# Optimization experiments

Hardware: AMD Instinct MI355X
Metric: run time of the kernel (lower is better)

Reference implementation:

```python
import jax, jax.numpy as jnp
import numpy as np

TOP_K = 2
B, S, H, I, E = 1, 2048, 1024, 4096, 8


def setup_inputs() -> dict:
    key = jax.random.key(0)
    k1, k2, k3, k4 = jax.random.split(key, 4)
    x = jax.random.normal(k1, (B, S, H), dtype=jnp.float32)
    gate_w = jax.random.normal(k2, (E, H), dtype=jnp.float32)
    w1 = jax.random.normal(k3, (E, I, H), dtype=jnp.float32)
    w2 = jax.random.normal(k4, (E, H, I), dtype=jnp.float32)
    return {"x": x, "gate_w": gate_w, "w1": w1, "w2": w2}


def reference(x, gate_w, w1, w2):
    b, s, h = x.shape
    xf = x.reshape(-1, h)                      # [T, H]
    T = xf.shape[0]
    logits = xf @ gate_w.T                     # [T, E]
    probs = jax.nn.softmax(logits, axis=-1)
    wts, idx = jax.lax.top_k(probs, TOP_K)     # [T, k]
    wts = wts / jnp.sum(wts, axis=-1, keepdims=True)
    # combine[t, e] = routing weight of expert e for token t (0 if not selected)
    combine = jnp.zeros((T, w1.shape[0]), dtype=x.dtype)
    combine = combine.at[jnp.arange(T)[:, None], idx].add(wts)
    # dense dispatch: every expert processes every token, masked/weighted by combine
    hid = jax.nn.silu(jnp.einsum('th,eih->tei', xf, w1))   # [T, E, I]
    y = jnp.einsum('tei,ehi->teh', hid, w2)                # [T, E, H]
    out = jnp.einsum('teh,te->th', y, combine)             # [T, H]
    return out.reshape(b, s, h)
```

## Files before the change

### kernel.cpp

```cpp
#include <hip/hip_runtime.h>
#include <stdint.h>

#define TT 2048
#define HH 1024
#define II 4096
#define EE 8
#define KS 4

typedef __attribute__((ext_vector_type(4))) float floatx4;
typedef __attribute__((ext_vector_type(8))) __bf16 bf16x8;

__device__ __forceinline__ unsigned short f2bf(float f) {
  union { float f; unsigned u; } v; v.f = f;
  return (unsigned short)((v.u + 0x7FFFu + ((v.u >> 16) & 1u)) >> 16);
}

__device__ __forceinline__ void async_ld16(const void* g, void* l) {
  __builtin_amdgcn_global_load_lds(
      (__attribute__((address_space(1))) void*)g,
      (__attribute__((address_space(3))) void*)l, 16, 0, 0);
}

__global__ __launch_bounds__(256) void k_gating(
    const float* __restrict__ x, const float* __restrict__ gw,
    unsigned short* __restrict__ xb, int* __restrict__ sel_e,
    float* __restrict__ sel_w, int* __restrict__ counts) {
  int t = blockIdx.x;
  int tid = threadIdx.x;
  floatx4 xv = ((const floatx4*)(x + (size_t)t * HH))[tid];
  ushort4 xo;
  xo.x = f2bf(xv.x); xo.y = f2bf(xv.y); xo.z = f2bf(xv.z); xo.w = f2bf(xv.w);
  ((ushort4*)(xb + (size_t)t * HH))[tid] = xo;

  float part[EE];
#pragma unroll
  for (int e = 0; e < EE; e++) {
    floatx4 g = ((const floatx4*)(gw + e * HH))[tid];
    part[e] = xv.x * g.x + xv.y * g.y + xv.z * g.z + xv.w * g.w;
  }
#pragma unroll
  for (int e = 0; e < EE; e++) {
    float v = part[e];
#pragma unroll
    for (int off = 32; off > 0; off >>= 1) v += __shfl_down(v, off, 64);
    part[e] = v;
  }
  __shared__ float red[4][EE];
  int wave = tid >> 6;
  if ((tid & 63) == 0) {
#pragma unroll
    for (int e = 0; e < EE; e++) red[wave][e] = part[e];
  }
  __syncthreads();
  if (tid == 0) {
    float lg[EE];
#pragma unroll
    for (int e = 0; e < EE; e++)
      lg[e] = red[0][e] + red[1][e] + red[2][e] + red[3][e];
    int e0 = 0;
#pragma unroll
    for (int e = 1; e < EE; e++) if (lg[e] > lg[e0]) e0 = e;
    int e1 = (e0 == 0) ? 1 : 0;
#pragma unroll
    for (int e = 0; e < EE; e++) if (e != e0 && lg[e] > lg[e1]) e1 = e;
    float w0 = 1.f / (1.f + expf(lg[e1] - lg[e0]));
    sel_e[t * 2] = e0; sel_e[t * 2 + 1] = e1;
    sel_w[t * 2] = w0; sel_w[t * 2 + 1] = 1.f - w0;
    atomicAdd(&counts[e0], 1);
    atomicAdd(&counts[e1], 1);
  }
}

__global__ __launch_bounds__(256) void k_fill(
    const int* __restrict__ counts, const int* __restrict__ sel_e,
    const float* __restrict__ sel_w, int* __restrict__ bases,
    int* __restrict__ row_token, float* __restrict__ row_w,
    int* __restrict__ inv_slot) {
  __shared__ int lb[EE];
  __shared__ int lc[EE];
  int tid = threadIdx.x;
  if (tid == 0) {
    int s = 0;
    for (int e = 0; e < EE; e++) { lb[e] = s; s += counts[e]; }
  }
  if (tid < EE) lc[tid] = 0;
  __syncthreads();
  for (int p = tid; p < TT * 2; p += 256) {
    int e = sel_e[p];
    int slot = lb[e] + atomicAdd(&lc[e], 1);
    row_token[slot] = p >> 1;
    row_w[slot] = sel_w[p];
    inv_slot[p] = slot;
  }
  __syncthreads();
  if (tid < EE) bases[tid] = lb[tid];
}

__global__ __launch_bounds__(256) void k_gemm1(
    const unsigned short* __restrict__ xb,
    const float* __restrict__ w1,
    unsigned short* __restrict__ hid,
    const int* __restrict__ counts, const int* __restrict__ bases,
    const int* __restrict__ row_token) {
  const int e = blockIdx.z;
  const int count = counts[e];
  const int m0 = blockIdx.y * 128;
  if (m0 >= count) return;
  const int n0 = blockIdx.x * 128;
  const int base = bases[e];

  __shared__ __align__(16) unsigned short Smem[128 * 32 * 2];
  unsigned short* As = Smem;
  unsigned short* Bs = Smem + 128 * 32;

  const int tid = threadIdx.x;
  const int lane = tid & 63;
  const int wave = tid >> 6;
  const int wm = (wave & 1) * 64;
  const int wn = (wave >> 1) * 64;
  const int quad = lane >> 4;
  const int l16 = lane & 15;

  const int rA0 = tid >> 2;
  const int rA1 = rA0 + 64;
  const int cc = (tid & 3) * 8;

  int g0 = m0 + rA0; if (g0 > count - 1) g0 = count - 1;
  int g1 = m0 + rA1; if (g1 > count - 1) g1 = count - 1;
  const unsigned short* aS0 = xb + (size_t)row_token[base + g0] * HH + cc;
  const unsigned short* aS1 = xb + (size_t)row_token[base + g1] * HH + cc;
  const float* wp = w1 + (size_t)e * II * HH;
  const float* bp0 = wp + (size_t)(n0 + rA0) * HH + cc;
  const float* bp1 = wp + (size_t)(n0 + rA1) * HH + cc;

  unsigned short* lA0 = As + tid * 8;
  unsigned short* lA1 = As + tid * 8 + 2048;
  unsigned short* lB0 = Bs + tid * 8;
  unsigned short* lB1 = Bs + tid * 8 + 2048;

  const floatx4 fz = {0.f, 0.f, 0.f, 0.f};
  floatx4 acc[4][4];
#pragma unroll
  for (int i = 0; i < 4; i++)
#pragma unroll
    for (int j = 0; j < 4; j++) acc[i][j] = fz;

  floatx4 f0a = *(const floatx4*)(bp0);
  floatx4 f0b = *(const floatx4*)(bp0 + 4);
  floatx4 f1a = *(const floatx4*)(bp1);
  floatx4 f1b = *(const floatx4*)(bp1 + 4);

  for (int k0 = 0; k0 < HH; k0 += 32) {
    bf16x8 wv0, wv1;
#pragma unroll
    for (int j = 0; j < 4; j++) {
      wv0[j] = (__bf16)f0a[j]; wv0[j + 4] = (__bf16)f0b[j];
      wv1[j] = (__bf16)f1a[j]; wv1[j + 4] = (__bf16)f1b[j];
    }
    *(bf16x8*)lB0 = wv0;
    *(bf16x8*)lB1 = wv1;
    async_ld16(aS0 + k0, lA0);
    async_ld16(aS1 + k0, lA1);
    __syncthreads();
    if (k0 + 32 < HH) {
      f0a = *(const floatx4*)(bp0 + k0 + 32);
      f0b = *(const floatx4*)(bp0 + k0 + 36);
      f1a = *(const floatx4*)(bp1 + k0 + 32);
      f1b = *(const floatx4*)(bp1 + k0 + 36);
    }
    bf16x8 af[4], bfr[4];
#pragma unroll
    for (int i = 0; i < 4; i++) {
      af[i]  = *(const bf16x8*)(As + (wm + i * 16 + l16) * 32 + quad * 8);
      bfr[i] = *(const bf16x8*)(Bs + (wn + i * 16 + l16) * 32 + quad * 8);
    }
#pragma unroll
    for (int i = 0; i < 4; i++)
#pragma unroll
      for (int j = 0; j < 4; j++)
        acc[i][j] = __builtin_amdgcn_mfma_f32_16x16x32_bf16(af[i], bfr[j], acc[i][j], 0, 0, 0);
    __syncthreads();
  }

  unsigned short* Sl = Smem + wave * (16 * 72);
#pragma unroll
  for (int i = 0; i < 4; i++) {
#pragma unroll
    for (int r = 0; r < 4; r++) {
      const int row16 = quad * 4 + r;
#pragma unroll
      for (int j = 0; j < 4; j++) {
        float z = acc[i][j][r];
        Sl[row16 * 72 + l16 + 16 * j] = f2bf(z / (1.f + __expf(-z)));
      }
    }
#pragma unroll
    for (int half = 0; half < 2; half++) {
      const int row16 = (lane >> 3) + 8 * half;
      const int m = wm + i * 16 + row16;
      if (m0 + m < count) {
        bf16x8 v = *(const bf16x8*)(Sl + row16 * 72 + (lane & 7) * 8);
        *(bf16x8*)(hid + (size_t)(base + m0 + m) * II + n0 + wn + (lane & 7) * 8) = v;
      }
    }
  }
}

__global__ __launch_bounds__(256) void k_gemm2(
    const unsigned short* __restrict__ hid,
    const float* __restrict__ w2,
    float* __restrict__ yp,
    const int* __restrict__ counts, const int* __restrict__ bases) {
  const int e = blockIdx.z;
  const int count = counts[e];
  const int m0 = blockIdx.y * 128;
  if (m0 >= count) return;
  const int nt = blockIdx.x & 7;
  const int ks = blockIdx.x >> 3;
  const int n0 = nt * 128;
  const int base = bases[e];

  __shared__ __align__(16) unsigned short Smem2[128 * 32 * 2];
  unsigned short* As = Smem2;
  unsigned short* Bs = Smem2 + 128 * 32;

  const int tid = threadIdx.x;
  const int lane = tid & 63;
  const int wave = tid >> 6;
  const int wm = (wave & 1) * 64;
  const int wn = (wave >> 1) * 64;
  const int quad = lane >> 4;
  const int l16 = lane & 15;

  const int rA0 = tid >> 2;
  const int rA1 = rA0 + 64;
  const int cc = (tid & 3) * 8;

  int g0 = m0 + rA0; if (g0 > count - 1) g0 = count - 1;
  int g1 = m0 + rA1; if (g1 > count - 1) g1 = count - 1;
  const unsigned short* aS0 = hid + (size_t)(base + g0) * II + cc;
  const unsigned short* aS1 = hid + (size_t)(base + g1) * II + cc;
  const float* wp = w2 + (size_t)e * HH * II;
  const float* bp0 = wp + (size_t)(n0 + rA0) * II + cc;
  const float* bp1 = wp + (size_t)(n0 + rA1) * II + cc;

  unsigned short* lA0 = As + tid * 8;
  unsigned short* lA1 = As + tid * 8 + 2048;
  unsigned short* lB0 = Bs + tid * 8;
  unsigned short* lB1 = Bs + tid * 8 + 2048;

  const floatx4 fz = {0.f, 0.f, 0.f, 0.f};
  floatx4 acc[4][4];
#pragma unroll
  for (int i = 0; i < 4; i++)
#pragma unroll
    for (int j = 0; j < 4; j++) acc[i][j] = fz;

  const int kbeg = ks * (II / KS);
  const int kend = kbeg + II / KS;

  floatx4 f0a = *(const floatx4*)(bp0 + kbeg);
  floatx4 f0b = *(const floatx4*)(bp0 + kbeg + 4);
  floatx4 f1a = *(const floatx4*)(bp1 + kbeg);
  floatx4 f1b = *(const floatx4*)(bp1 + kbeg + 4);

  for (int k0 = kbeg; k0 < kend; k0 += 32) {
    bf16x8 wv0, wv1;
#pragma unroll
    for (int j = 0; j < 4; j++) {
      wv0[j] = (__bf16)f0a[j]; wv0[j + 4] = (__bf16)f0b[j];
      wv1[j] = (__bf16)f1a[j]; wv1[j + 4] = (__bf16)f1b[j];
    }
    *(bf16x8*)lB0 = wv0;
    *(bf16x8*)lB1 = wv1;
    async_ld16(aS0 + k0, lA0);
    async_ld16(aS1 + k0, lA1);
    __syncthreads();
    if (k0 + 32 < kend) {
      f0a = *(const floatx4*)(bp0 + k0 + 32);
      f0b = *(const floatx4*)(bp0 + k0 + 36);
      f1a = *(const floatx4*)(bp1 + k0 + 32);
      f1b = *(const floatx4*)(bp1 + k0 + 36);
    }
    bf16x8 af[4], bfr[4];
#pragma unroll
    for (int i = 0; i < 4; i++) {
      af[i]  = *(const bf16x8*)(As + (wm + i * 16 + l16) * 32 + quad * 8);
      bfr[i] = *(const bf16x8*)(Bs + (wn + i * 16 + l16) * 32 + quad * 8);
    }
#pragma unroll
    for (int i = 0; i < 4; i++)
#pragma unroll
      for (int j = 0; j < 4; j++)
        acc[i][j] = __builtin_amdgcn_mfma_f32_16x16x32_bf16(af[i], bfr[j], acc[i][j], 0, 0, 0);
    __syncthreads();
  }

#pragma unroll
  for (int i = 0; i < 4; i++) {
#pragma unroll
    for (int r = 0; r < 4; r++) {
      const int m = wm + i * 16 + quad * 4 + r;
      if (m0 + m < count) {
        float* op = yp + ((size_t)ks * (TT * 2) + base + m0 + m) * HH + n0 + wn + l16;
#pragma unroll
        for (int j = 0; j < 4; j++) op[j * 16] = acc[i][j][r];
      }
    }
  }
}

__global__ __launch_bounds__(256) void k_combine(
    const float* __restrict__ yp, const int* __restrict__ inv_slot,
    const float* __restrict__ sel_w, float* __restrict__ out) {
  const int t = blockIdx.x;
  const int tid = threadIdx.x;
  const int s0 = inv_slot[2 * t];
  const int s1 = inv_slot[2 * t + 1];
  const float w0 = sel_w[2 * t];
  const float w1 = sel_w[2 * t + 1];
  floatx4 a = {0.f, 0.f, 0.f, 0.f};
  floatx4 b = {0.f, 0.f, 0.f, 0.f};
#pragma unroll
  for (int ks = 0; ks < KS; ks++) {
    a += ((const floatx4*)(yp + ((size_t)ks * (TT * 2) + s0) * HH))[tid];
    b += ((const floatx4*)(yp + ((size_t)ks * (TT * 2) + s1) * HH))[tid];
  }
  floatx4 v = w0 * a + w1 * b;
  ((floatx4*)(out + (size_t)t * HH))[tid] = v;
}

extern "C" void kernel_launch(void* const* d_in, const int* in_sizes, int n_in,
                              void* d_out, int out_size, void* d_ws, size_t ws_size,
                              hipStream_t stream) {
  const float* x  = (const float*)d_in[0];
  const float* gw = (const float*)d_in[1];
  const float* w1 = (const float*)d_in[2];
  const float* w2 = (const float*)d_in[3];
  float* out = (float*)d_out;

  char* ws = (char*)d_ws;
  size_t off = 0;
  auto take = [&](size_t n) -> char* {
    char* p = ws + off;
    off += (n + 255) & ~(size_t)255;
    return p;
  };
  unsigned short* xb  = (unsigned short*)take((size_t)TT * HH * 2);
  unsigned short* hid = (unsigned short*)take((size_t)TT * 2 * II * 2);
  float* yp = (float*)take((size_t)KS * (TT * 2) * HH * 4);
  int*   counts    = (int*)take(EE * 4);
  int*   bases     = (int*)take(EE * 4);
  int*   row_token = (int*)take((size_t)TT * 2 * 4);
  float* row_w     = (float*)take((size_t)TT * 2 * 4);
  int*   sel_e     = (int*)take((size_t)TT * 2 * 4);
  float* sel_w     = (float*)take((size_t)TT * 2 * 4);
  int*   inv_slot  = (int*)take((size_t)TT * 2 * 4);
  if (off > ws_size) return;

  hipMemsetAsync(counts, 0, EE * 4, stream);

  k_gating<<<TT, 256, 0, stream>>>(x, gw, xb, sel_e, sel_w, counts);
  k_fill<<<1, 256, 0, stream>>>(counts, sel_e, sel_w, bases, row_token, row_w, inv_slot);
  k_gemm1<<<dim3(II / 128, 16, EE), 256, 0, stream>>>(xb, w1, hid, counts, bases, row_token);
  k_gemm2<<<dim3(8 * KS, 16, EE), 256, 0, stream>>>(hid, w2, yp, counts, bases);
  k_combine<<<TT, 256, 0, stream>>>(yp, inv_slot, sel_w, out);
}
```

Measured before the change: 469.8 us.

## Double-buffer GEMM LDS tiles, swizzle LDS layout, fuse combine via atomics

Both expert GEMMs now keep two LDS buffers, so the next k-tile's global loads overlap the current tile's MFMA work, with one barrier per iteration instead of two. The LDS layout is XOR-swizzled to reduce bank conflicts on fragment reads. The separate combine kernel and its split-K partial buffer are removed: gemm2 atomically adds weighted results straight into a zeroed output. This saves the partial-buffer traffic and one launch, at the cost of float atomic contention and non-deterministic summation order.

After: 493.6 us. 5.1% more time.

```diff
diff --git a/kernel.cpp b/kernel.cpp
--- a/kernel.cpp
+++ b/kernel.cpp
@@ -6,6 +6,7 @@
 #define II 4096
 #define EE 8
 #define KS 4
+#define KSPAN (II / KS)
 
 typedef __attribute__((ext_vector_type(4))) float floatx4;
 typedef __attribute__((ext_vector_type(8))) __bf16 bf16x8;
@@ -20,6 +21,10 @@
       (__attribute__((address_space(1))) void*)g,
       (__attribute__((address_space(3))) void*)l, 16, 0, 0);
 }
+
+#define CFENCE asm volatile("" ::: "memory")
+#define WAIT_VM(n) asm volatile("s_waitcnt vmcnt(" #n ")" ::: "memory")
+#define WAIT_LGKM0 asm volatile("s_waitcnt lgkmcnt(0)" ::: "memory")
 
 __global__ __launch_bounds__(256) void k_gating(
     const float* __restrict__ x, const float* __restrict__ gw,
@@ -74,8 +79,7 @@
 __global__ __launch_bounds__(256) void k_fill(
     const int* __restrict__ counts, const int* __restrict__ sel_e,
     const float* __restrict__ sel_w, int* __restrict__ bases,
-    int* __restrict__ row_token, float* __restrict__ row_w,
-    int* __restrict__ inv_slot) {
+    int* __restrict__ row_token, float* __restrict__ row_w) {
   __shared__ int lb[EE];
   __shared__ int lc[EE];
   int tid = threadIdx.x;
@@ -90,7 +94,6 @@
     int slot = lb[e] + atomicAdd(&lc[e], 1);
     row_token[slot] = p >> 1;
     row_w[slot] = sel_w[p];
-    inv_slot[p] = slot;
   }
   __syncthreads();
   if (tid < EE) bases[tid] = lb[tid];
@@ -109,9 +112,11 @@
   const int n0 = blockIdx.x * 128;
   const int base = bases[e];
 
-  __shared__ __align__(16) unsigned short Smem[128 * 32 * 2];
-  unsigned short* As = Smem;
-  unsigned short* Bs = Smem + 128 * 32;
+  __shared__ __align__(16) unsigned short Smem[4 * 4096];
+  unsigned short* const A0b = Smem;
+  unsigned short* const A1b = Smem + 4096;
+  unsigned short* const B0b = Smem + 8192;
+  unsigned short* const B1b = Smem + 12288;
 
   const int tid = threadIdx.x;
   const int lane = tid & 63;
@@ -122,21 +127,28 @@
   const int l16 = lane & 15;
 
   const int rA0 = tid >> 2;
-  const int rA1 = rA0 + 64;
-  const int cc = (tid & 3) * 8;
-
-  int g0 = m0 + rA0; if (g0 > count - 1) g0 = count - 1;
-  int g1 = m0 + rA1; if (g1 > count - 1) g1 = count - 1;
-  const unsigned short* aS0 = xb + (size_t)row_token[base + g0] * HH + cc;
-  const unsigned short* aS1 = xb + (size_t)row_token[base + g1] * HH + cc;
+  const int swz = (tid & 3) ^ ((tid >> 3) & 3);
+  const int ccA = swz * 8;
+  const int ccB = (tid & 3) * 8;
+  const int ldsA = tid * 8;
+  const int ldsB = rA0 * 32 + swz * 8;
+
+  int g0 = m0 + rA0;      if (g0 > count - 1) g0 = count - 1;
+  int g1 = m0 + rA0 + 64; if (g1 > count - 1) g1 = count - 1;
+  const unsigned short* aS0 = xb + (size_t)row_token[base + g0] * HH + ccA;
+  const unsigned short* aS1 = xb + (size_t)row_token[base + g1] * HH + ccA;
   const float* wp = w1 + (size_t)e * II * HH;
-  const float* bp0 = wp + (size_t)(n0 + rA0) * HH + cc;
-  const float* bp1 = wp + (size_t)(n0 + rA1) * HH + cc;
-
-  unsigned short* lA0 = As + tid * 8;
-  unsigned short* lA1 = As + tid * 8 + 2048;
-  unsigned short* lB0 = Bs + tid * 8;
-  unsigned short* lB1 = Bs + tid * 8 + 2048;
+  const float* bp0 = wp + (size_t)(n0 + rA0) * HH + ccB;
+  const float* bp1 = bp0 + (size_t)64 * HH;
+
+  int offA[4], offB[4];
+#pragma unroll
+  for (int i = 0; i < 4; i++) {
+    const int Ra = wm + i * 16 + l16;
+    offA[i] = Ra * 32 + 8 * (quad ^ ((Ra >> 1) & 3));
+    const int Rb = wn + i * 16 + l16;
+    offB[i] = Rb * 32 + 8 * (quad ^ ((Rb >> 1) & 3));
+  }
 
   const floatx4 fz = {0.f, 0.f, 0.f, 0.f};
   floatx4 acc[4][4];
@@ -145,41 +157,72 @@
 #pragma unroll
     for (int j = 0; j < 4; j++) acc[i][j] = fz;
 
-  floatx4 f0a = *(const floatx4*)(bp0);
-  floatx4 f0b = *(const floatx4*)(bp0 + 4);
-  floatx4 f1a = *(const floatx4*)(bp1);
-  floatx4 f1b = *(const floatx4*)(bp1 + 4);
-
-  for (int k0 = 0; k0 < HH; k0 += 32) {
+  {
+    floatx4 f0a = *(const floatx4*)(bp0);
+    floatx4 f0b = *(const floatx4*)(bp0 + 4);
+    floatx4 f1a = *(const floatx4*)(bp1);
+    floatx4 f1b = *(const floatx4*)(bp1 + 4);
+    CFENCE;
+    async_ld16(aS0, A0b + ldsA);
+    async_ld16(aS1, A0b + ldsA + 2048);
+    CFENCE;
+    WAIT_VM(2);
     bf16x8 wv0, wv1;
 #pragma unroll
     for (int j = 0; j < 4; j++) {
       wv0[j] = (__bf16)f0a[j]; wv0[j + 4] = (__bf16)f0b[j];
       wv1[j] = (__bf16)f1a[j]; wv1[j + 4] = (__bf16)f1b[j];
     }
-    *(bf16x8*)lB0 = wv0;
-    *(bf16x8*)lB1 = wv1;
-    async_ld16(aS0 + k0, lA0);
-    async_ld16(aS1 + k0, lA1);
-    __syncthreads();
-    if (k0 + 32 < HH) {
-      f0a = *(const floatx4*)(bp0 + k0 + 32);
-      f0b = *(const floatx4*)(bp0 + k0 + 36);
-      f1a = *(const floatx4*)(bp1 + k0 + 32);
-      f1b = *(const floatx4*)(bp1 + k0 + 36);
+    *(bf16x8*)(B0b + ldsB) = wv0;
+    *(bf16x8*)(B0b + ldsB + 2048) = wv1;
+    WAIT_VM(0);
+    WAIT_LGKM0;
+    __builtin_amdgcn_s_barrier();
+  }
+
+  unsigned short* Ac = A0b; unsigned short* An = A1b;
+  unsigned short* Bc = B0b; unsigned short* Bn = B1b;
+
+  for (int k0 = 0; k0 < HH; k0 += 32) {
+    const bool has1 = (k0 + 32 < HH);
+    floatx4 g0a, g0b, g1a, g1b;
+    if (has1) {
+      g0a = *(const floatx4*)(bp0 + k0 + 32);
+      g0b = *(const floatx4*)(bp0 + k0 + 36);
+      g1a = *(const floatx4*)(bp1 + k0 + 32);
+      g1b = *(const floatx4*)(bp1 + k0 + 36);
+      CFENCE;
+      async_ld16(aS0 + k0 + 32, An + ldsA);
+      async_ld16(aS1 + k0 + 32, An + ldsA + 2048);
+      CFENCE;
     }
     bf16x8 af[4], bfr[4];
 #pragma unroll
     for (int i = 0; i < 4; i++) {
-      af[i]  = *(const bf16x8*)(As + (wm + i * 16 + l16) * 32 + quad * 8);
-      bfr[i] = *(const bf16x8*)(Bs + (wn + i * 16 + l16) * 32 + quad * 8);
+      af[i]  = *(const bf16x8*)(Ac + offA[i]);
+      bfr[i] = *(const bf16x8*)(Bc + offB[i]);
     }
 #pragma unroll
     for (int i = 0; i < 4; i++)
 #pragma unroll
       for (int j = 0; j < 4; j++)
         acc[i][j] = __builtin_amdgcn_mfma_f32_16x16x32_bf16(af[i], bfr[j], acc[i][j], 0, 0, 0);
-    __syncthreads();
+    if (has1) {
+      WAIT_VM(2);
+      bf16x8 wv0, wv1;
+#pragma unroll
+      for (int j = 0; j < 4; j++) {
+        wv0[j] = (__bf16)g0a[j]; wv0[j + 4] = (__bf16)g0b[j];
+        wv1[j] = (__bf16)g1a[j]; wv1[j + 4] = (__bf16)g1b[j];
+      }
+      *(bf16x8*)(Bn + ldsB) = wv0;
+      *(bf16x8*)(Bn + ldsB + 2048) = wv1;
+      WAIT_VM(0);
+    }
+    WAIT_LGKM0;
+    __builtin_amdgcn_s_barrier();
+    { unsigned short* t = Ac; Ac = An; An = t; }
+    { unsigned short* t = Bc; Bc = Bn; Bn = t; }
   }
 
   unsigned short* Sl = Smem + wave * (16 * 72);
@@ -209,8 +252,9 @@
 __global__ __launch_bounds__(256) void k_gemm2(
     const unsigned short* __restrict__ hid,
     const float* __restrict__ w2,
-    float* __restrict__ yp,
-    const int* __restrict__ counts, const int* __restrict__ bases) {
+    float* __restrict__ out,
+    const int* __restrict__ counts, const int* __restrict__ bases,
+    const int* __restrict__ row_token, const float* __restrict__ row_w) {
   const int e = blockIdx.z;
   const int count = counts[e];
   const int m0 = blockIdx.y * 128;
@@ -219,10 +263,13 @@
   const int ks = blockIdx.x >> 3;
   const int n0 = nt * 128;
   const int base = bases[e];
-
-  __shared__ __align__(16) unsigned short Smem2[128 * 32 * 2];
-  unsigned short* As = Smem2;
-  unsigned short* Bs = Smem2 + 128 * 32;
+  const int kbeg = ks * KSPAN;
+
+  __shared__ __align__(16) unsigned short Smem2[4 * 4096];
+  unsigned short* const A0b = Smem2;
+  unsigned short* const A1b = Smem2 + 4096;
+  unsigned short* const B0b = Smem2 + 8192;
+  unsigned short* const B1b = Smem2 + 12288;
 
   const int tid = threadIdx.x;
   const int lane = tid & 63;
@@ -233,21 +280,28 @@
   const int l16 = lane & 15;
 
   const int rA0 = tid >> 2;
-  const int rA1 = rA0 + 64;
-  const int cc = (tid & 3) * 8;
-
-  int g0 = m0 + rA0; if (g0 > count - 1) g0 = count - 1;
-  int g1 = m0 + rA1; if (g1 > count - 1) g1 = count - 1;
-  const unsigned short* aS0 = hid + (size_t)(base + g0) * II + cc;
-  const unsigned short* aS1 = hid + (size_t)(base + g1) * II + cc;
+  const int swz = (tid & 3) ^ ((tid >> 3) & 3);
+  const int ccA = swz * 8;
+  const int ccB = (tid & 3) * 8;
+  const int ldsA = tid * 8;
+  const int ldsB = rA0 * 32 + swz * 8;
+
+  int g0 = m0 + rA0;      if (g0 > count - 1) g0 = count - 1;
+  int g1 = m0 + rA0 + 64; if (g1 > count - 1) g1 = count - 1;
+  const unsigned short* aS0 = hid + (size_t)(base + g0) * II + kbeg + ccA;
+  const unsigned short* aS1 = hid + (size_t)(base + g1) * II + kbeg + ccA;
   const float* wp = w2 + (size_t)e * HH * II;
-  const float* bp0 = wp + (size_t)(n0 + rA0) * II + cc;
-  const float* bp1 = wp + (size_t)(n0 + rA1) * II + cc;
-
-  unsigned short* lA0 = As + tid * 8;
-  unsigned short* lA1 = As + tid * 8 + 2048;
-  unsigned short* lB0 = Bs + tid * 8;
-  unsigned short* lB1 = Bs + tid * 8 + 2048;
+  const float* bp0 = wp + (size_t)(n0 + rA0) * II + kbeg + ccB;
+  const float* bp1 = bp0 + (size_t)64 * II;
+
+  int offA[4], offB[4];
+#pragma unroll
+  for (int i = 0; i < 4; i++) {
+    const int Ra = wm + i * 16 + l16;
+    offA[i] = Ra * 32 + 8 * (quad ^ ((Ra >> 1) & 3));
+    const int Rb = wn + i * 16 + l16;
+    offB[i] = Rb * 32 + 8 * (quad ^ ((Rb >> 1) & 3));
+  }
 
   const floatx4 fz = {0.f, 0.f, 0.f, 0.f};
   floatx4 acc[4][4];
@@ -256,44 +310,72 @@
 #pragma unroll
     for (int j = 0; j < 4; j++) acc[i][j] = fz;
 
-  const int kbeg = ks * (II / KS);
-  const int kend = kbeg + II / KS;
-
-  floatx4 f0a = *(const floatx4*)(bp0 + kbeg);
-  floatx4 f0b = *(const floatx4*)(bp0 + kbeg + 4);
-  floatx4 f1a = *(const floatx4*)(bp1 + kbeg);
-  floatx4 f1b = *(const floatx4*)(bp1 + kbeg + 4);
-
-  for (int k0 = kbeg; k0 < kend; k0 += 32) {
+  {
+    floatx4 f0a = *(const floatx4*)(bp0);
+    floatx4 f0b = *(const floatx4*)(bp0 + 4);
+    floatx4 f1a = *(const floatx4*)(bp1);
+    floatx4 f1b = *(const floatx4*)(bp1 + 4);
+    CFENCE;
+    async_ld16(aS0, A0b + ldsA);
+    async_ld16(aS1, A0b + ldsA + 2048);
+    CFENCE;
+    WAIT_VM(2);
     bf16x8 wv0, wv1;
 #pragma unroll
     for (int j = 0; j < 4; j++) {
       wv0[j] = (__bf16)f0a[j]; wv0[j + 4] = (__bf16)f0b[j];
       wv1[j] = (__bf16)f1a[j]; wv1[j + 4] = (__bf16)f1b[j];
     }
-    *(bf16x8*)lB0 = wv0;
-    *(bf16x8*)lB1 = wv1;
-    async_ld16(aS0 + k0, lA0);
-    async_ld16(aS1 + k0, lA1);
-    __syncthreads();
-    if (k0 + 32 < kend) {
-      f0a = *(const floatx4*)(bp0 + k0 + 32);
-      f0b = *(const floatx4*)(bp0 + k0 + 36);
-      f1a = *(const floatx4*)(bp1 + k0 + 32);
-      f1b = *(const floatx4*)(bp1 + k0 + 36);
+    *(bf16x8*)(B0b + ldsB) = wv0;
+    *(bf16x8*)(B0b + ldsB + 2048) = wv1;
+    WAIT_VM(0);
+    WAIT_LGKM0;
+    __builtin_amdgcn_s_barrier();
+  }
+
+  unsigned short* Ac = A0b; unsigned short* An = A1b;
+  unsigned short* Bc = B0b; unsigned short* Bn = B1b;
+
+  for (int k0 = 0; k0 < KSPAN; k0 += 32) {
+    const bool has1 = (k0 + 32 < KSPAN);
+    floatx4 g0a, g0b, g1a, g1b;
+    if (has1) {
+      g0a = *(const floatx4*)(bp0 + k0 + 32);
+      g0b = *(const floatx4*)(bp0 + k0 + 36);
+      g1a = *(const floatx4*)(bp1 + k0 + 32);
+      g1b = *(const floatx4*)(bp1 + k0 + 36);
+      CFENCE;
+      async_ld16(aS0 + k0 + 32, An + ldsA);
+      async_ld16(aS1 + k0 + 32, An + ldsA + 2048);
+      CFENCE;
     }
     bf16x8 af[4], bfr[4];
 #pragma unroll
     for (int i = 0; i < 4; i++) {
-      af[i]  = *(const bf16x8*)(As + (wm + i * 16 + l16) * 32 + quad * 8);
-      bfr[i] = *(const bf16x8*)(Bs + (wn + i * 16 + l16) * 32 + quad * 8);
+      af[i]  = *(const bf16x8*)(Ac + offA[i]);
+      bfr[i] = *(const bf16x8*)(Bc + offB[i]);
     }
 #pragma unroll
     for (int i = 0; i < 4; i++)
 #pragma unroll
       for (int j = 0; j < 4; j++)
         acc[i][j] = __builtin_amdgcn_mfma_f32_16x16x32_bf16(af[i], bfr[j], acc[i][j], 0, 0, 0);
-    __syncthreads();
+    if (has1) {
+      WAIT_VM(2);
+      bf16x8 wv0, wv1;
+#pragma unroll
+      for (int j = 0; j < 4; j++) {
+        wv0[j] = (__bf16)g0a[j]; wv0[j + 4] = (__bf16)g0b[j];
+        wv1[j] = (__bf16)g1a[j]; wv1[j + 4] = (__bf16)g1b[j];
+      }
+      *(bf16x8*)(Bn + ldsB) = wv0;
+      *(bf16x8*)(Bn + ldsB + 2048) = wv1;
+      WAIT_VM(0);
+    }
+    WAIT_LGKM0;
+    __builtin_amdgcn_s_barrier();
+    { unsigned short* t = Ac; Ac = An; An = t; }
+    { unsigned short* t = Bc; Bc = Bn; Bn = t; }
   }
 
 #pragma unroll
@@ -302,32 +384,15 @@
     for (int r = 0; r < 4; r++) {
       const int m = wm + i * 16 + quad * 4 + r;
       if (m0 + m < count) {
-        float* op = yp + ((size_t)ks * (TT * 2) + base + m0 + m) * HH + n0 + wn + l16;
-#pragma unroll
-        for (int j = 0; j < 4; j++) op[j * 16] = acc[i][j][r];
+        const int slot = base + m0 + m;
+        const int tok = row_token[slot];
+        const float wgt = row_w[slot];
+        float* op = out + (size_t)tok * HH + n0 + wn + l16;
+#pragma unroll
+        for (int j = 0; j < 4; j++) atomicAdd(op + j * 16, wgt * acc[i][j][r]);
       }
     }
   }
-}
-
-__global__ __launch_bounds__(256) void k_combine(
-    const float* __restrict__ yp, const int* __restrict__ inv_slot,
-    const float* __restrict__ sel_w, float* __restrict__ out) {
-  const int t = blockIdx.x;
-  const int tid = threadIdx.x;
-  const int s0 = inv_slot[2 * t];
-  const int s1 = inv_slot[2 * t + 1];
-  const float w0 = sel_w[2 * t];
-  const float w1 = sel_w[2 * t + 1];
-  floatx4 a = {0.f, 0.f, 0.f, 0.f};
-  floatx4 b = {0.f, 0.f, 0.f, 0.f};
-#pragma unroll
-  for (int ks = 0; ks < KS; ks++) {
-    a += ((const floatx4*)(yp + ((size_t)ks * (TT * 2) + s0) * HH))[tid];
-    b += ((const floatx4*)(yp + ((size_t)ks * (TT * 2) + s1) * HH))[tid];
-  }
-  floatx4 v = w0 * a + w1 * b;
-  ((floatx4*)(out + (size_t)t * HH))[tid] = v;
 }
 
 extern "C" void kernel_launch(void* const* d_in, const int* in_sizes, int n_in,
@@ -348,21 +413,19 @@
   };
   unsigned short* xb  = (unsigned short*)take((size_t)TT * HH * 2);
   unsigned short* hid = (unsigned short*)take((size_t)TT * 2 * II * 2);
-  float* yp = (float*)take((size_t)KS * (TT * 2) * HH * 4);
   int*   counts    = (int*)take(EE * 4);
   int*   bases     = (int*)take(EE * 4);
   int*   row_token = (int*)take((size_t)TT * 2 * 4);
   float* row_w     = (float*)take((size_t)TT * 2 * 4);
   int*   sel_e     = (int*)take((size_t)TT * 2 * 4);
   float* sel_w     = (float*)take((size_t)TT * 2 * 4);
-  int*   inv_slot  = (int*)take((size_t)TT * 2 * 4);
   if (off > ws_size) return;
 
   hipMemsetAsync(counts, 0, EE * 4, stream);
+  hipMemsetAsync(out, 0, (size_t)TT * HH * 4, stream);
 
   k_gating<<<TT, 256, 0, stream>>>(x, gw, xb, sel_e, sel_w, counts);
-  k_fill<<<1, 256, 0, stream>>>(counts, sel_e, sel_w, bases, row_token, row_w, inv_slot);
+  k_fill<<<1, 256, 0, stream>>>(counts, sel_e, sel_w, bases, row_token, row_w);
   k_gemm1<<<dim3(II / 128, 16, EE), 256, 0, stream>>>(xb, w1, hid, counts, bases, row_token);
-  k_gemm2<<<dim3(8 * KS, 16, EE), 256, 0, stream>>>(hid, w2, yp, counts, bases);
-  k_combine<<<TT, 256, 0, stream>>>(yp, inv_slot, sel_w, out);
-}
+  k_gemm2<<<dim3(8 * KS, 16, EE), 256, 0, stream>>>(hid, w2, out, counts, bases, row_token, row_w);
+}
```
